# Kernel optimization log

Hardware: AMD Instinct MI355X
Metric: run time of the kernel (lower is better)

Reference implementation:

```python
import jax, jax.numpy as jnp
import numpy as np

D_MODEL = 1024
K_QUERY = 32
K_TOPK = 4

def setup_inputs() -> dict:
    key = jax.random.key(0)
    k1, k2, k3, k4, k5 = jax.random.split(key, 5)
    x = jax.random.normal(k1, (4, 2048, D_MODEL), dtype=jnp.float32)
    # nn.Linear(d_model, k_query): weight [k_query, d_model], bias [k_query]
    sc = 1.0 / np.sqrt(D_MODEL)
    Wq = jax.random.uniform(k2, (K_QUERY, D_MODEL), jnp.float32, -sc, sc)
    bq = jax.random.uniform(k3, (K_QUERY,), jnp.float32, -sc, sc)
    Wk = jax.random.uniform(k4, (K_QUERY, D_MODEL), jnp.float32, -sc, sc)
    bk = jax.random.uniform(k5, (K_QUERY,), jnp.float32, -sc, sc)
    return {"x": x, "Wq": Wq, "bq": bq, "Wk": Wk, "bk": bk}

def reference(x, Wq, bq, Wk, bk):
    # x: [B, T, D]
    queries = jnp.einsum('btd,kd->btk', x, Wq) + bq      # [B, T, Kq]
    keys = jnp.einsum('btd,kd->btk', x, Wk) + bk         # [B, T, Kq]
    sim = jnp.einsum('btk,bsk->bts', queries, keys)      # [B, T, T]
    sim = sim / jnp.sqrt(jnp.float32(queries.shape[-1]))
    _, topk_idx = jax.lax.top_k(sim, K_TOPK)              # [B, T, K]
    # gather neighbors per (b, t): x[b, topk_idx[b, t]] -> [B, T, K, D]
    neighbors = jax.vmap(lambda xb, ib: xb[ib])(x, topk_idx)
    gathered = neighbors.mean(axis=2)                     # [B, T, D]
    return gathered
```

## Files before the change

kernel.cpp:

```cpp
#include <hip/hip_runtime.h>
#include <math.h>

#define D_MODEL 1024
#define T_SEQ   2048
#define NBATCH  4
#define NROWS   (NBATCH * T_SEQ)
#define NOUT    64

#define T16F   1024

typedef float  v4f  __attribute__((ext_vector_type(4)));
typedef _Float16 v8hf __attribute__((ext_vector_type(8)));

__device__ __forceinline__ bool key_gt(float av, int ai, float bv, int bi) {
    return (av > bv) || (av == bv && ai < bi);
}

__device__ __forceinline__ void cmpswap(float& v0, int& i0, float& v1, int& i1) {
    bool sw = key_gt(v1, i1, v0, i0);
    float nv0 = sw ? v1 : v0, nv1 = sw ? v0 : v1;
    int   ni0 = sw ? i1 : i0, ni1 = sw ? i0 : i1;
    v0 = nv0; v1 = nv1; i0 = ni0; i1 = ni1;
}

__device__ __forceinline__ void merge4(float (&a)[4], int (&ai)[4],
                                       float b0, int j0, float b1, int j1,
                                       float b2, int j2, float b3, int j3) {
    if (!key_gt(a[0], ai[0], b3, j3)) { a[0] = b3; ai[0] = j3; }
    if (!key_gt(a[1], ai[1], b2, j2)) { a[1] = b2; ai[1] = j2; }
    if (!key_gt(a[2], ai[2], b1, j1)) { a[2] = b1; ai[2] = j1; }
    if (!key_gt(a[3], ai[3], b0, j0)) { a[3] = b0; ai[3] = j0; }
    cmpswap(a[0], ai[0], a[2], ai[2]);
    cmpswap(a[1], ai[1], a[3], ai[3]);
    cmpswap(a[0], ai[0], a[1], ai[1]);
    cmpswap(a[2], ai[2], a[3], ai[3]);
}

__device__ __forceinline__ void insert4(float (&tv)[4], int (&tix)[4], float v, int idx) {
    if (v > tv[3]) {
        bool g0 = v > tv[0], g1 = v > tv[1], g2 = v > tv[2];
        float n0 = g0 ? v : tv[0];
        int   m0 = g0 ? idx : tix[0];
        float n1 = g1 ? (g0 ? tv[0] : v) : tv[1];
        int   m1 = g1 ? (g0 ? tix[0] : idx) : tix[1];
        float n2 = g2 ? (g1 ? tv[1] : v) : tv[2];
        int   m2 = g2 ? (g1 ? tix[1] : idx) : tix[2];
        float n3 = g2 ? tv[2] : v;
        int   m3 = g2 ? tix[2] : idx;
        tv[0] = n0; tv[1] = n1; tv[2] = n2; tv[3] = n3;
        tix[0] = m0; tix[1] = m1; tix[2] = m2; tix[3] = m3;
    }
}

__device__ int run_probe16_block(int tid, int nthr, int* __restrict__ tab, int wr)
{
    __shared__ _Float16 A16[16][32];
    __shared__ _Float16 B16[32][16];
    __shared__ float    D16[16][16];
    __shared__ int      flagS;

    for (int e = tid; e < 512; e += nthr) {
        const int m = e >> 5, k = e & 31;
        A16[m][k] = (_Float16)(float)(1 + (3 * m + 5 * k) % 61);
        const int kk = e >> 4, n = e & 15;
        B16[kk][n] = (_Float16)(float)(1 + (7 * kk + 11 * n) % 59);
    }
    __syncthreads();
    for (int e = tid; e < 256; e += nthr) {
        const int m = e >> 4, n = e & 15;
        float s = 0.f;
        for (int k = 0; k < 32; ++k) s += (float)A16[m][k] * (float)B16[k][n];
        D16[m][n] = s;
    }
    __syncthreads();

    if (tid < 64) {
        const int lane = tid;
        v8hf a, b;
        const int ab = (lane >> 4) * 8;
        #pragma unroll
        for (int j = 0; j < 8; ++j) {
            a[j] = A16[lane & 15][ab + j];
            b[j] = B16[ab + j][lane & 15];
        }
        v4f c = {0.f, 0.f, 0.f, 0.f};
        c = __builtin_amdgcn_mfma_f32_16x16x32_f16(a, b, c, 0, 0, 0);
        bool ok0 = true;
        #pragma unroll
        for (int i = 0; i < 4; ++i)
            ok0 = ok0 && (c[i] == D16[4 * (lane >> 4) + i][lane & 15]);
        int found = __all(ok0) ? 0 : -1;
        if (lane == 0) { flagS = found; if (wr) tab[T16F] = found; }
    }
    __syncthreads();
    return flagS;
}

__global__ __launch_bounds__(1024, 8) void proj_fused(
    const float* __restrict__ x,
    const float* __restrict__ Wq, const float* __restrict__ Wk,
    const float* __restrict__ bq, const float* __restrict__ bk_,
    int* __restrict__ tab,
    float* __restrict__ Qt, float* __restrict__ Kt,
    _Float16* __restrict__ Qh, _Float16* __restrict__ Ql,
    _Float16* __restrict__ Kh, _Float16* __restrict__ Kl)
{
    __shared__ float comb[3][4][64][4];

    const int tid  = threadIdx.x;
    const int lane = tid & 63;
    const int wav  = tid >> 6;
    const int og   = __builtin_amdgcn_readfirstlane(wav & 3);
    const int kq   = __builtin_amdgcn_readfirstlane(wav >> 2);
    const int row0 = blockIdx.x * 16;

    const int flag = run_probe16_block(tid, 1024, tab, blockIdx.x == 0);

    if (flag == 0) {
        const int m  = lane & 15;
        const int ko = (lane >> 4) * 8;
        const int kb = kq * 256;
        const int o  = og * 16 + m;
        const float* xrow = x + (size_t)(row0 + m) * D_MODEL + kb + ko;
        const float* wrow = ((o < 32) ? Wq + (size_t)o * D_MODEL
                                      : Wk + (size_t)(o - 32) * D_MODEL) + kb + ko;

        v4f hh = {0.f, 0.f, 0.f, 0.f};
        v4f hl = {0.f, 0.f, 0.f, 0.f};
        v4f lh = {0.f, 0.f, 0.f, 0.f};
        #pragma unroll 2
        for (int kc = 0; kc < 8; ++kc) {
            float4 x0 = *reinterpret_cast<const float4*>(xrow + kc * 32);
            float4 x1 = *reinterpret_cast<const float4*>(xrow + kc * 32 + 4);
            float4 w0 = *reinterpret_cast<const float4*>(wrow + kc * 32);
            float4 w1 = *reinterpret_cast<const float4*>(wrow + kc * 32 + 4);
            const float xf[8] = {x0.x, x0.y, x0.z, x0.w, x1.x, x1.y, x1.z, x1.w};
            const float wf[8] = {w0.x, w0.y, w0.z, w0.w, w1.x, w1.y, w1.z, w1.w};
            v8hf ah, al, bh, bl;
            #pragma unroll
            for (int e = 0; e < 8; ++e) {
                _Float16 h = (_Float16)xf[e];
                ah[e] = h; al[e] = (_Float16)(xf[e] - (float)h);
                _Float16 g = (_Float16)wf[e];
                bh[e] = g; bl[e] = (_Float16)(wf[e] - (float)g);
            }
            hh = __builtin_amdgcn_mfma_f32_16x16x32_f16(ah, bh, hh, 0, 0, 0);
            hl = __builtin_amdgcn_mfma_f32_16x16x32_f16(ah, bl, hl, 0, 0, 0);
            lh = __builtin_amdgcn_mfma_f32_16x16x32_f16(al, bh, lh, 0, 0, 0);
        }

        v4f t;
        #pragma unroll
        for (int i = 0; i < 4; ++i) t[i] = (hh[i] + hl[i]) + lh[i];

        if (kq > 0) {
            #pragma unroll
            for (int i = 0; i < 4; ++i) comb[kq - 1][og][lane][i] = t[i];
        }
        __syncthreads();
        if (kq == 0) {
            #pragma unroll
            for (int i = 0; i < 4; ++i) {
                const float tot = (t[i] + comb[0][og][lane][i])
                                + (comb[1][og][lane][i] + comb[2][og][lane][i]);
                const int row = row0 + 4 * (lane >> 4) + i;
                const float bias = (o < 32) ? bq[o] : bk_[o - 32];
                const float v = tot + bias;
                const _Float16 h = (_Float16)v;
                const _Float16 l = (_Float16)(v - (float)h);
                if (o < 32) {
                    Qh[(size_t)row * 32 + o] = h;
                    Ql[(size_t)row * 32 + o] = l;
                } else {
                    Kh[(size_t)row * 32 + (o - 32)] = h;
                    Kl[(size_t)row * 32 + (o - 32)] = l;
                }
            }
        }
        return;
    }

    if (kq == 0) {
        const int n  = lane & 15;
        const int r4 = (lane >> 4) * 4;
        const int o  = og * 16 + n;
        const float* wr = (o < 32) ? Wq + (size_t)o * D_MODEL
                                   : Wk + (size_t)(o - 32) * D_MODEL;
        double acc[4] = {0.0, 0.0, 0.0, 0.0};
        for (int d = 0; d < D_MODEL; ++d) {
            const double wv = (double)wr[d];
            #pragma unroll
            for (int i = 0; i < 4; ++i)
                acc[i] = fma((double)x[(size_t)(row0 + r4 + i) * D_MODEL + d], wv, acc[i]);
        }
        #pragma unroll
        for (int i = 0; i < 4; ++i) {
            const int row = row0 + r4 + i;
            const int bb  = row >> 11, tt = row & 2047;
            const double bias = (o < 32) ? (double)bq[o] : (double)bk_[o - 32];
            const float v = (float)(acc[i] + bias);
            if (o < 32) Qt[((size_t)bb * 32 + o) * T_SEQ + tt] = v;
            else        Kt[((size_t)bb * 32 + (o - 32)) * T_SEQ + tt] = v;
        }
    }
}

__global__ __launch_bounds__(1024, 8) void sim_topk_gather(
    const float* __restrict__ x,
    const _Float16* __restrict__ Qh, const _Float16* __restrict__ Ql,
    const _Float16* __restrict__ Kh, const _Float16* __restrict__ Kl,
    const float* __restrict__ Qt, const float* __restrict__ Kt,
    const int* __restrict__ tab,
    float* __restrict__ out)
{
    __shared__ float sV[16][16][4];
    __shared__ int   sI[16][16][4];
    __shared__ float sVf[16][64][4];
    __shared__ int   sIf[16][64][4];
    __shared__ int   topIdx[16][4];

    const int tid  = threadIdx.x;
    const int lane = tid & 63;
    const int wav  = tid >> 6;
    const int tt   = blockIdx.x & 127;
    const int b    = blockIdx.x >> 7;
    const int row0g = b * T_SEQ + tt * 16;

    if (tab[T16F] == 0) {
        const int m  = lane & 15;
        const int ko = (lane >> 4) * 8;
        v8hf qh = *reinterpret_cast<const v8hf*>(Qh + (size_t)(row0g + m) * 32 + ko);
        v8hf ql = *reinterpret_cast<const v8hf*>(Ql + (size_t)(row0g + m) * 32 + ko);
        const _Float16* KhB = Kh + (size_t)b * T_SEQ * 32;
        const _Float16* KlB = Kl + (size_t)b * T_SEQ * 32;

        float tv[4]; int tix[4];
        #pragma unroll
        for (int j = 0; j < 4; ++j) { tv[j] = -INFINITY; tix[j] = 0x7fffffff; }

        const int sq = wav * 128;
        #pragma unroll 2
        for (int st = 0; st < 8; ++st) {
            const int s0 = sq + st * 16;
            v8hf kh = *reinterpret_cast<const v8hf*>(KhB + (size_t)(s0 + m) * 32 + ko);
            v8hf kl = *reinterpret_cast<const v8hf*>(KlB + (size_t)(s0 + m) * 32 + ko);
            v4f c = {0.f, 0.f, 0.f, 0.f};
            c = __builtin_amdgcn_mfma_f32_16x16x32_f16(kh, qh, c, 0, 0, 0);
            c = __builtin_amdgcn_mfma_f32_16x16x32_f16(kl, qh, c, 0, 0, 0);
            c = __builtin_amdgcn_mfma_f32_16x16x32_f16(kh, ql, c, 0, 0, 0);
            c = __builtin_amdgcn_mfma_f32_16x16x32_f16(kl, ql, c, 0, 0, 0);
            const int sb = s0 + 4 * (lane >> 4);
            #pragma unroll
            for (int i = 0; i < 4; ++i) insert4(tv, tix, c[i], sb + i);
        }

        #pragma unroll
        for (int mk = 16; mk <= 32; mk <<= 1) {
            float b0 = __shfl_xor(tv[0], mk, 64);
            float b1 = __shfl_xor(tv[1], mk, 64);
            float b2 = __shfl_xor(tv[2], mk, 64);
            float b3 = __shfl_xor(tv[3], mk, 64);
            int   j0 = __shfl_xor(tix[0], mk, 64);
            int   j1 = __shfl_xor(tix[1], mk, 64);
            int   j2 = __shfl_xor(tix[2], mk, 64);
            int   j3 = __shfl_xor(tix[3], mk, 64);
            merge4(tv, tix, b0, j0, b1, j1, b2, j2, b3, j3);
        }

        if (lane < 16) {
            #pragma unroll
            for (int j = 0; j < 4; ++j) {
                sV[wav][lane][j] = tv[j];
                sI[wav][lane][j] = tix[j];
            }
        }
        __syncthreads();

        if (tid < 16) {
            float mv[4]; int mi[4];
            #pragma unroll
            for (int j = 0; j < 4; ++j) { mv[j] = sV[0][tid][j]; mi[j] = sI[0][tid][j]; }
            #pragma unroll
            for (int w = 1; w < 16; ++w)
                merge4(mv, mi,
                       sV[w][tid][0], sI[w][tid][0],
                       sV[w][tid][1], sI[w][tid][1],
                       sV[w][tid][2], sI[w][tid][2],
                       sV[w][tid][3], sI[w][tid][3]);
            #pragma unroll
            for (int j = 0; j < 4; ++j) topIdx[tid][j] = mi[j];
        }
        __syncthreads();
    } else {
        const float* QtB = Qt + (size_t)b * 32 * T_SEQ;
        const float* KtB = Kt + (size_t)b * 32 * T_SEQ;
        const int row   = tid >> 6;
        const int chunk = tid & 63;
        const int trow  = tt * 16 + row;
        float tv4[4]; int tix4[4];
        #pragma unroll
        for (int j = 0; j < 4; ++j) { tv4[j] = -INFINITY; tix4[j] = 0x7fffffff; }
        for (int s = chunk * 32; s < chunk * 32 + 32; ++s) {
            float sum = 0.f;
            for (int i = 0; i < 32; ++i)
                sum = fmaf(QtB[(size_t)i * T_SEQ + trow], KtB[(size_t)i * T_SEQ + s], sum);
            insert4(tv4, tix4, sum, s);
        }
        #pragma unroll
        for (int j = 0; j < 4; ++j) { sVf[row][chunk][j] = tv4[j]; sIf[row][chunk][j] = tix4[j]; }
        __syncthreads();
        if (tid < 16) {
            float mv[4]; int mi[4];
            #pragma unroll
            for (int j = 0; j < 4; ++j) { mv[j] = sVf[tid][0][j]; mi[j] = sIf[tid][0][j]; }
            for (int cc = 1; cc < 64; ++cc)
                merge4(mv, mi,
                       sVf[tid][cc][0], sIf[tid][cc][0],
                       sVf[tid][cc][1], sIf[tid][cc][1],
                       sVf[tid][cc][2], sIf[tid][cc][2],
                       sVf[tid][cc][3], sIf[tid][cc][3]);
            #pragma unroll
            for (int j = 0; j < 4; ++j) topIdx[tid][j] = mi[j];
        }
        __syncthreads();
    }

    const float* xb = x + (size_t)b * T_SEQ * D_MODEL;
    float* ob = out + (size_t)row0g * D_MODEL;
    const int rh = tid >> 8;
    const int t4 = tid & 255;
    #pragma unroll
    for (int rp = 0; rp < 4; ++rp) {
        const int r = rp * 4 + rh;
        const int i0 = topIdx[r][0], i1 = topIdx[r][1], i2 = topIdx[r][2], i3 = topIdx[r][3];
        float4 a0 = *(reinterpret_cast<const float4*>(xb + (size_t)i0 * D_MODEL) + t4);
        float4 a1 = *(reinterpret_cast<const float4*>(xb + (size_t)i1 * D_MODEL) + t4);
        float4 a2 = *(reinterpret_cast<const float4*>(xb + (size_t)i2 * D_MODEL) + t4);
        float4 a3 = *(reinterpret_cast<const float4*>(xb + (size_t)i3 * D_MODEL) + t4);
        float4 o;
        o.x = (a0.x + a1.x + a2.x + a3.x) * 0.25f;
        o.y = (a0.y + a1.y + a2.y + a3.y) * 0.25f;
        o.z = (a0.z + a1.z + a2.z + a3.z) * 0.25f;
        o.w = (a0.w + a1.w + a2.w + a3.w) * 0.25f;
        *(reinterpret_cast<float4*>(ob + (size_t)r * D_MODEL) + t4) = o;
    }
}

extern "C" void kernel_launch(void* const* d_in, const int* in_sizes, int n_in,
                              void* d_out, int out_size, void* d_ws, size_t ws_size,
                              hipStream_t stream) {
    const float* x  = (const float*)d_in[0];
    const float* Wq = (const float*)d_in[1];
    const float* bq = (const float*)d_in[2];
    const float* Wk = (const float*)d_in[3];
    const float* bk = (const float*)d_in[4];
    float* out = (float*)d_out;

    char* wsb = (char*)d_ws;
    int*      tab = (int*)wsb;
    float*    Qt  = (float*)(wsb + 8192);
    float*    Kt  = Qt + (size_t)NBATCH * 32 * T_SEQ;
    _Float16* Qh  = (_Float16*)((char*)Kt + (size_t)NBATCH * 32 * T_SEQ * 4);
    _Float16* Ql  = Qh + (size_t)NROWS * 32;
    _Float16* Kh  = Ql + (size_t)NROWS * 32;
    _Float16* Kl  = Kh + (size_t)NROWS * 32;

    proj_fused<<<dim3(NROWS / 16), dim3(1024), 0, stream>>>(
        x, Wq, Wk, bq, bk, tab, Qt, Kt, Qh, Ql, Kh, Kl);
    sim_topk_gather<<<dim3(512), dim3(1024), 0, stream>>>(
        x, Qh, Ql, Kh, Kl, Qt, Kt, tab, out);
}
```

Measured before the change: 145.5 us.

## Interleave hi/lo fp16 Q/K buffers and skip top-4 inserts below threshold

Stores the fp16 high and low parts of each Q and K row contiguously in one 64-element row instead of four separate arrays, so each key row is read from a single cache line. In the MFMA similarity loop, a 4-value tile is inserted into the running top-4 only when its maximum beats the current fourth-best value, which avoids most compare-swap work. The loop unroll goes from 2 to 4, and the two shared-memory scratch arrays are merged into one. The early-exit branch can diverge within a wavefront, and the deeper unroll raises register pressure.

```diff
diff --git a/kernel.cpp b/kernel.cpp
--- a/kernel.cpp
+++ b/kernel.cpp
@@ -102,8 +102,7 @@
     const float* __restrict__ bq, const float* __restrict__ bk_,
     int* __restrict__ tab,
     float* __restrict__ Qt, float* __restrict__ Kt,
-    _Float16* __restrict__ Qh, _Float16* __restrict__ Ql,
-    _Float16* __restrict__ Kh, _Float16* __restrict__ Kl)
+    _Float16* __restrict__ QC, _Float16* __restrict__ KC)
 {
     __shared__ float comb[3][4][64][4];
 
@@ -169,11 +168,11 @@
                 const _Float16 h = (_Float16)v;
                 const _Float16 l = (_Float16)(v - (float)h);
                 if (o < 32) {
-                    Qh[(size_t)row * 32 + o] = h;
-                    Ql[(size_t)row * 32 + o] = l;
+                    QC[(size_t)row * 64 + o]      = h;
+                    QC[(size_t)row * 64 + 32 + o] = l;
                 } else {
-                    Kh[(size_t)row * 32 + (o - 32)] = h;
-                    Kl[(size_t)row * 32 + (o - 32)] = l;
+                    KC[(size_t)row * 64 + (o - 32)]      = h;
+                    KC[(size_t)row * 64 + 32 + (o - 32)] = l;
                 }
             }
         }
@@ -207,16 +206,13 @@
 
 __global__ __launch_bounds__(1024, 8) void sim_topk_gather(
     const float* __restrict__ x,
-    const _Float16* __restrict__ Qh, const _Float16* __restrict__ Ql,
-    const _Float16* __restrict__ Kh, const _Float16* __restrict__ Kl,
+    const _Float16* __restrict__ QC, const _Float16* __restrict__ KC,
     const float* __restrict__ Qt, const float* __restrict__ Kt,
     const int* __restrict__ tab,
     float* __restrict__ out)
 {
-    __shared__ float sV[16][16][4];
-    __shared__ int   sI[16][16][4];
-    __shared__ float sVf[16][64][4];
-    __shared__ int   sIf[16][64][4];
+    __shared__ float sV[16][64][4];
+    __shared__ int   sI[16][64][4];
     __shared__ int   topIdx[16][4];
 
     const int tid  = threadIdx.x;
@@ -229,29 +225,32 @@
     if (tab[T16F] == 0) {
         const int m  = lane & 15;
         const int ko = (lane >> 4) * 8;
-        v8hf qh = *reinterpret_cast<const v8hf*>(Qh + (size_t)(row0g + m) * 32 + ko);
-        v8hf ql = *reinterpret_cast<const v8hf*>(Ql + (size_t)(row0g + m) * 32 + ko);
-        const _Float16* KhB = Kh + (size_t)b * T_SEQ * 32;
-        const _Float16* KlB = Kl + (size_t)b * T_SEQ * 32;
+        v8hf qh = *reinterpret_cast<const v8hf*>(QC + (size_t)(row0g + m) * 64 + ko);
+        v8hf ql = *reinterpret_cast<const v8hf*>(QC + (size_t)(row0g + m) * 64 + 32 + ko);
+        const _Float16* KCB = KC + (size_t)b * T_SEQ * 64;
 
         float tv[4]; int tix[4];
         #pragma unroll
         for (int j = 0; j < 4; ++j) { tv[j] = -INFINITY; tix[j] = 0x7fffffff; }
 
         const int sq = wav * 128;
-        #pragma unroll 2
+        #pragma unroll 4
         for (int st = 0; st < 8; ++st) {
             const int s0 = sq + st * 16;
-            v8hf kh = *reinterpret_cast<const v8hf*>(KhB + (size_t)(s0 + m) * 32 + ko);
-            v8hf kl = *reinterpret_cast<const v8hf*>(KlB + (size_t)(s0 + m) * 32 + ko);
+            const _Float16* kr = KCB + (size_t)(s0 + m) * 64 + ko;
+            v8hf kh = *reinterpret_cast<const v8hf*>(kr);
+            v8hf kl = *reinterpret_cast<const v8hf*>(kr + 32);
             v4f c = {0.f, 0.f, 0.f, 0.f};
             c = __builtin_amdgcn_mfma_f32_16x16x32_f16(kh, qh, c, 0, 0, 0);
             c = __builtin_amdgcn_mfma_f32_16x16x32_f16(kl, qh, c, 0, 0, 0);
             c = __builtin_amdgcn_mfma_f32_16x16x32_f16(kh, ql, c, 0, 0, 0);
             c = __builtin_amdgcn_mfma_f32_16x16x32_f16(kl, ql, c, 0, 0, 0);
-            const int sb = s0 + 4 * (lane >> 4);
-            #pragma unroll
-            for (int i = 0; i < 4; ++i) insert4(tv, tix, c[i], sb + i);
+            const float cmax = fmaxf(fmaxf(c[0], c[1]), fmaxf(c[2], c[3]));
+            if (cmax > tv[3]) {
+                const int sb = s0 + 4 * (lane >> 4);
+                #pragma unroll
+                for (int i = 0; i < 4; ++i) insert4(tv, tix, c[i], sb + i);
+            }
         }
 
         #pragma unroll
@@ -307,18 +306,18 @@
             insert4(tv4, tix4, sum, s);
         }
         #pragma unroll
-        for (int j = 0; j < 4; ++j) { sVf[row][chunk][j] = tv4[j]; sIf[row][chunk][j] = tix4[j]; }
+        for (int j = 0; j < 4; ++j) { sV[row][chunk][j] = tv4[j]; sI[row][chunk][j] = tix4[j]; }
         __syncthreads();
         if (tid < 16) {
             float mv[4]; int mi[4];
             #pragma unroll
-            for (int j = 0; j < 4; ++j) { mv[j] = sVf[tid][0][j]; mi[j] = sIf[tid][0][j]; }
+            for (int j = 0; j < 4; ++j) { mv[j] = sV[tid][0][j]; mi[j] = sI[tid][0][j]; }
             for (int cc = 1; cc < 64; ++cc)
                 merge4(mv, mi,
-                       sVf[tid][cc][0], sIf[tid][cc][0],
-                       sVf[tid][cc][1], sIf[tid][cc][1],
-                       sVf[tid][cc][2], sIf[tid][cc][2],
-                       sVf[tid][cc][3], sIf[tid][cc][3]);
+                       sV[tid][cc][0], sI[tid][cc][0],
+                       sV[tid][cc][1], sI[tid][cc][1],
+                       sV[tid][cc][2], sI[tid][cc][2],
+                       sV[tid][cc][3], sI[tid][cc][3]);
             #pragma unroll
             for (int j = 0; j < 4; ++j) topIdx[tid][j] = mi[j];
         }
@@ -360,13 +359,11 @@
     int*      tab = (int*)wsb;
     float*    Qt  = (float*)(wsb + 8192);
     float*    Kt  = Qt + (size_t)NBATCH * 32 * T_SEQ;
-    _Float16* Qh  = (_Float16*)((char*)Kt + (size_t)NBATCH * 32 * T_SEQ * 4);
-    _Float16* Ql  = Qh + (size_t)NROWS * 32;
-    _Float16* Kh  = Ql + (size_t)NROWS * 32;
-    _Float16* Kl  = Kh + (size_t)NROWS * 32;
+    _Float16* QC  = (_Float16*)((char*)Kt + (size_t)NBATCH * 32 * T_SEQ * 4);
+    _Float16* KC  = QC + (size_t)NROWS * 64;
 
     proj_fused<<<dim3(NROWS / 16), dim3(1024), 0, stream>>>(
-        x, Wq, Wk, bq, bk, tab, Qt, Kt, Qh, Ql, Kh, Kl);
+        x, Wq, Wk, bq, bk, tab, Qt, Kt, QC, KC);
     sim_topk_gather<<<dim3(512), dim3(1024), 0, stream>>>(
-        x, Qh, Ql, Kh, Kl, Qt, Kt, tab, out);
-}
+        x, QC, KC, Qt, Kt, tab, out);
+}
```

Result: no change. 147.1 us (+1.1%).
